# Kernel tuning notes

Measured on AMD Instinct MI355X. Metric: run time of the kernel, lower is better.

## Reference

```python
import jax, jax.numpy as jnp
import numpy as np

SX = 512; SY = 512; C = 3; NK = 10; R = 10
DT = 0.2; DD = 5; SIGMA = 0.65; THETA_A = 1.0; NPOW = 2


def setup_inputs() -> dict:
    rng = np.random.RandomState(0)
    r = rng.uniform(0.3, 1.0, NK).astype(np.float32)
    m = rng.uniform(0.05, 0.5, NK).astype(np.float32)
    s = rng.uniform(0.01, 0.18, NK).astype(np.float32)
    h = rng.uniform(0.2, 1.0, NK).astype(np.float32)
    a = rng.uniform(0.0, 1.0, (NK, 3)).astype(np.float32)
    w = rng.uniform(0.01, 0.5, (NK, 3)).astype(np.float32)
    b = rng.uniform(0.0, 1.0, (NK, 3)).astype(np.float32)
    # compute_kernel(): radial distance grid, ring sigmoid * sum-of-bumps ker_f, normalized
    mid = SX // 2
    x = np.linspace(-mid, mid, 2 * mid, dtype=np.float32)
    X, Y = np.meshgrid(x, x, indexing='ij')
    dist = np.sqrt(X ** 2 + Y ** 2)
    D = dist[:, :, None] / ((R + 15.0) * r)                      # (SX, SY, NK)
    ring = 1.0 / (1.0 + np.exp((D - 1.0) * 10.0))                # sigmoid(-(D-1)*10)
    bumps = (b * np.exp(-((D[..., None] - a) ** 2) / w)).sum(-1)  # ker_f(D, a, w, b)
    K = (ring * bumps).astype(np.float32)
    nK_ker = K / K.sum(axis=(0, 1), keepdims=True)               # (SX, SY, NK)
    # kernel -> source channel, and kernel -> target channel one-hot (c1 as matrix)
    c0 = np.array([0, 0, 0, 1, 1, 1, 2, 2, 2, 0], dtype=np.int32)
    tgt = np.array([0, 1, 2, 0, 1, 2, 0, 1, 2, 0], dtype=np.int32)
    c1_mat = np.zeros((NK, C), dtype=np.int32)
    c1_mat[np.arange(NK), tgt] = 1
    key = jax.random.key(0)
    A = jax.random.uniform(key, (SX, SY, C), dtype=jnp.float32)  # scale_init_state = 1
    return {"A": A, "nK_ker": jnp.asarray(nK_ker), "m": jnp.asarray(m),
            "s": jnp.asarray(s), "h": jnp.asarray(h),
            "c0": jnp.asarray(c0), "c1_mat": jnp.asarray(c1_mat)}


def _sobel(A):
    """A: (SX, SY, Cc) -> (SX, SY, 2, Cc), circular (toroidal) boundary."""
    def grad_ax(ax):
        sm_ax = 1 - ax
        sm = jnp.roll(A, 1, sm_ax) + 2.0 * A + jnp.roll(A, -1, sm_ax)  # [1,2,1] smoothing
        return (jnp.roll(sm, -1, ax) - jnp.roll(sm, 1, ax)) / 8.0       # central diff
    return jnp.stack([grad_ax(0), grad_ax(1)], axis=2)


def _flowlenia_step(A, nK_ker, m, s, h, c0, c1_mat):
    # FFT Lenia convolution
    fA = jnp.fft.fft2(A, axes=(0, 1))                              # (SX, SY, C) complex
    fK = jnp.fft.fft2(jnp.fft.fftshift(nK_ker, axes=(0, 1)), axes=(0, 1))
    U = jnp.real(jnp.fft.ifft2(fK * fA[:, :, c0], axes=(0, 1)))    # (SX, SY, NK)
    # growth * h, then gather-sum kernels into target channels (c1)
    U = (2.0 * jnp.exp(-((U - m) ** 2) / (2.0 * s ** 2)) - 1.0) * h
    U = jnp.einsum('xyk,kc->xyc', U, c1_mat.astype(U.dtype))       # (SX, SY, C)
    # flow field
    nabla_U = _sobel(U)                                            # (SX, SY, 2, C)
    nabla_A = _sobel(A.sum(-1, keepdims=True))                     # (SX, SY, 2, 1)
    alpha = jnp.clip((A[:, :, None, :] / THETA_A) ** NPOW, 0.0, 1.0)
    F = nabla_U * (1.0 - alpha) - nabla_A * alpha                  # (SX, SY, 2, C)
    # reintegration tracking (mass-conserving advection over (2*DD+1)^2 shifts)
    xs = jnp.arange(SX, dtype=A.dtype)
    ys = jnp.arange(SY, dtype=A.dtype)
    X, Y = jnp.meshgrid(xs, ys, indexing='ij')
    pos = jnp.stack([X, Y], axis=-1) + 0.5                         # (SX, SY, 2) cell centers
    ma = DD - SIGMA                                                # max flow magnitude
    mu = pos[..., None] + DT * jnp.clip(F, -ma, ma)                # (SX, SY, 2, C)
    shifts = jnp.array([(dx, dy) for dx in range(-DD, DD + 1)
                        for dy in range(-DD, DD + 1)], dtype=jnp.int32)
    clip_hi = min(1.0, 2.0 * SIGMA)
    inv_norm = 1.0 / (4.0 * SIGMA ** 2)

    def body(acc, sh):
        dx, dy = sh[0], sh[1]
        rA = jnp.roll(jnp.roll(A, dx, 0), dy, 1)
        rmu = jnp.roll(jnp.roll(mu, dx, 0), dy, 1)
        sz = 0.5 - jnp.abs(pos[..., None] - rmu) + SIGMA
        area = jnp.prod(jnp.clip(sz, 0.0, clip_hi), axis=2) * inv_norm  # (SX, SY, C)
        return acc + rA * area, None

    nA, _ = jax.lax.scan(body, jnp.zeros_like(A), shifts)
    return nA


def reference(A, nK_ker, m, s, h, c0, c1_mat):
    return _flowlenia_step(A, nK_ker, m, s, h, c0, c1_mat)
```

## Files before the change

### kernel.cpp

```cpp
#include <hip/hip_runtime.h>
#include <math.h>

#define NF 512
#define NF2 (NF * NF)
#define RPB 4
#define ROWLEN 580
#define PI_F 3.14159265358979323846f

#define LPAD(q) ((q) + ((q) >> 3))

__device__ inline float2 cadd(float2 a, float2 b) { return make_float2(a.x + b.x, a.y + b.y); }
__device__ inline float2 csub(float2 a, float2 b) { return make_float2(a.x - b.x, a.y - b.y); }
__device__ inline float2 cmul(float2 a, float2 b) {
    return make_float2(a.x * b.x - a.y * b.y, a.x * b.y + a.y * b.x);
}

__device__ inline void fft8(float2 x[8], float dsign) {
    const float s = 0.70710678118654752440f;
    float2 a0 = cadd(x[0], x[4]), a1 = cadd(x[1], x[5]);
    float2 a2 = cadd(x[2], x[6]), a3 = cadd(x[3], x[7]);
    float2 b0 = csub(x[0], x[4]), b1 = csub(x[1], x[5]);
    float2 b2 = csub(x[2], x[6]), b3 = csub(x[3], x[7]);
    b1 = cmul(b1, make_float2(s, dsign * s));
    b2 = make_float2(-dsign * b2.y, dsign * b2.x);
    b3 = cmul(b3, make_float2(-s, dsign * s));
    float2 c0 = cadd(a0, a2), c1 = cadd(a1, a3);
    float2 c2 = csub(a0, a2), c3 = csub(a1, a3);
    c3 = make_float2(-dsign * c3.y, dsign * c3.x);
    float2 d0 = cadd(b0, b2), d1 = cadd(b1, b3);
    float2 d2 = csub(b0, b2), d3 = csub(b1, b3);
    d3 = make_float2(-dsign * d3.y, dsign * d3.x);
    x[0] = cadd(c0, c1); x[4] = csub(c0, c1);
    x[2] = cadd(c2, c3); x[6] = csub(c2, c3);
    x[1] = cadd(d0, d1); x[5] = csub(d0, d1);
    x[3] = cadd(d2, d3); x[7] = csub(d2, d3);
}

__device__ inline void twiddle8(float2 x[8], float2 wb) {
    float2 tw = wb;
    x[1] = cmul(x[1], tw); tw = cmul(tw, wb);
    x[2] = cmul(x[2], tw); tw = cmul(tw, wb);
    x[3] = cmul(x[3], tw); tw = cmul(tw, wb);
    x[4] = cmul(x[4], tw); tw = cmul(tw, wb);
    x[5] = cmul(x[5], tw); tw = cmul(tw, wb);
    x[6] = cmul(x[6], tw); tw = cmul(tw, wb);
    x[7] = cmul(x[7], tw);
}

__device__ inline void fft512_regs(float2 x[8], int b, float2* bufA, float2* bufB,
                                   const float2* Wt, float dsign) {
    fft8(x, dsign);
    float2 wb0 = make_float2(Wt[b].x, dsign * Wt[b].y);
    twiddle8(x, wb0);
#pragma unroll
    for (int p = 0; p < 8; ++p) bufA[9 * b + p] = x[p];
    __syncthreads();
#pragma unroll
    for (int j = 0; j < 8; ++j) x[j] = bufA[LPAD(b + 64 * j)];
    fft8(x, dsign);
    int u = b >> 3, v = b & 7;
    float2 wb1 = make_float2(Wt[b & ~7].x, dsign * Wt[b & ~7].y);
    twiddle8(x, wb1);
    int base = u * 64 + v;
#pragma unroll
    for (int p = 0; p < 8; ++p) bufB[LPAD(base + 8 * p)] = x[p];
    __syncthreads();
#pragma unroll
    for (int j = 0; j < 8; ++j) x[j] = bufB[LPAD(b + 64 * j)];
    fft8(x, dsign);
}

#define FFT_PRE                                                    \
    __shared__ float2 SHA[RPB][ROWLEN];                            \
    __shared__ float2 SHB[RPB][ROWLEN];                            \
    __shared__ float2 Wt[512];                                     \
    int tid = threadIdx.x;                                         \
    int rr_ = tid >> 6, bb_ = tid & 63;                            \
    {                                                              \
        float sn, cs;                                              \
        sincosf((PI_F / 256.0f) * (float)tid, &sn, &cs);           \
        Wt[tid] = make_float2(cs, sn);                             \
        sincosf((PI_F / 256.0f) * (float)(tid + 256), &sn, &cs);   \
        Wt[tid + 256] = make_float2(cs, sn);                       \
    }

__device__ inline float2 unpack_field(const float2* __restrict__ Z, int plane, int slot,
                                      int ky, int kx) {
    const float2* P = Z + (size_t)plane * NF2;
    float2 zr = P[(ky << 9) + kx];
    float2 zm = P[(((NF - ky) & (NF - 1)) << 9) + ((NF - kx) & (NF - 1))];
    if (slot == 0)
        return make_float2(0.5f * (zr.x + zm.x), 0.5f * (zr.y - zm.y));
    else
        return make_float2(0.5f * (zr.y + zm.y), 0.5f * (zm.x - zr.x));
}

__global__ __launch_bounds__(256) void k_fwd_p1(const float* __restrict__ A,
                                                const float* __restrict__ K,
                                                float2* __restrict__ Z) {
    FFT_PRE
    int pl = blockIdx.y;
    const float* bre; int sre, cre;
    const float* bim; int sim, cim;
    switch (pl) {
        case 0: bre = A; sre = 3; cre = 0; bim = A; sim = 3; cim = 1; break;
        case 1: bre = A; sre = 3; cre = 2; bim = K; sim = 10; cim = 0; break;
        case 2: bre = K; sre = 10; cre = 1; bim = K; sim = 10; cim = 2; break;
        case 3: bre = K; sre = 10; cre = 3; bim = K; sim = 10; cim = 4; break;
        case 4: bre = K; sre = 10; cre = 5; bim = K; sim = 10; cim = 6; break;
        case 5: bre = K; sre = 10; cre = 7; bim = K; sim = 10; cim = 8; break;
        default: bre = K; sre = 10; cre = 9; bim = nullptr; sim = 0; cim = 0; break;
    }
    int x0 = blockIdx.x * RPB;
    int row = x0 + rr_;
    float2 x[8];
#pragma unroll
    for (int j = 0; j < 8; ++j) {
        int idx = (row << 9) + bb_ + 64 * j;
        float vr = bre[idx * sre + cre];
        float vi = bim ? bim[idx * sim + cim] : 0.0f;
        x[j] = make_float2(vr, vi);
    }
    __syncthreads();
    fft512_regs(x, bb_, &SHA[rr_][0], &SHB[rr_][0], Wt, -1.0f);
#pragma unroll
    for (int p2 = 0; p2 < 8; ++p2) SHA[rr_][LPAD(64 * p2 + bb_)] = x[p2];
    __syncthreads();
    for (int i = tid; i < RPB * NF; i += 256) {
        int r2 = i & (RPB - 1), ky = i >> 2;
        Z[(size_t)((pl << 9) + ky) * NF + x0 + r2] = SHA[r2][LPAD(ky)];
    }
}

__global__ __launch_bounds__(256) void k_fft_rows(float2* __restrict__ data, float dsign) {
    FFT_PRE
    int R0 = blockIdx.x * RPB;
    size_t rowbase = (size_t)(R0 + rr_) * NF;
    float2 x[8];
#pragma unroll
    for (int j = 0; j < 8; ++j) x[j] = data[rowbase + bb_ + 64 * j];
    __syncthreads();
    fft512_regs(x, bb_, &SHA[rr_][0], &SHB[rr_][0], Wt, dsign);
#pragma unroll
    for (int p2 = 0; p2 < 8; ++p2) SHA[rr_][LPAD(64 * p2 + bb_)] = x[p2];
    __syncthreads();
    for (int i = tid; i < RPB * NF; i += 256) {
        int r2 = i >> 9, xx = i & (NF - 1);
        data[(size_t)(R0 + r2) * NF + xx] = SHA[r2][LPAD(xx)];
    }
}

__global__ __launch_bounds__(256) void k_mulinv_p1(const float2* __restrict__ Z,
                                                   const int* __restrict__ c0,
                                                   float2* __restrict__ tmp) {
    FFT_PRE
    int jp = blockIdx.y;
    int k1 = 2 * jp, k2 = 2 * jp + 1;
    int pK1 = (k1 == 0) ? 1 : 2 + ((k1 - 1) >> 1);
    int sK1 = (k1 == 0) ? 1 : ((k1 - 1) & 1);
    int pK2 = 2 + ((k2 - 1) >> 1);
    int sK2 = (k2 - 1) & 1;
    int cA1 = c0[k1], cA2 = c0[k2];
    int pA1 = cA1 >> 1, sA1 = cA1 & 1;
    int pA2 = cA2 >> 1, sA2 = cA2 & 1;
    bool sameA = (cA1 == cA2);

    int ky0 = blockIdx.x * RPB;
    int ky = ky0 + rr_;
    float2 x[8];
#pragma unroll
    for (int jj = 0; jj < 8; ++jj) {
        int kx = bb_ + 64 * jj;
        float2 fk1 = unpack_field(Z, pK1, sK1, ky, kx);
        float2 fk2 = unpack_field(Z, pK2, sK2, ky, kx);
        float2 fa1 = unpack_field(Z, pA1, sA1, ky, kx);
        float2 fa2 = sameA ? fa1 : unpack_field(Z, pA2, sA2, ky, kx);
        float t1x = fk1.x * fa1.x - fk1.y * fa1.y;
        float t1y = fk1.x * fa1.y + fk1.y * fa1.x;
        float t2x = fk2.x * fa2.x - fk2.y * fa2.y;
        float t2y = fk2.x * fa2.y + fk2.y * fa2.x;
        float sgn = ((kx + ky) & 1) ? -1.0f : 1.0f;
        x[jj] = make_float2((t1x - t2y) * sgn, (t1y + t2x) * sgn);
    }
    __syncthreads();
    fft512_regs(x, bb_, &SHA[rr_][0], &SHB[rr_][0], Wt, +1.0f);
#pragma unroll
    for (int p2 = 0; p2 < 8; ++p2) SHA[rr_][LPAD(64 * p2 + bb_)] = x[p2];
    __syncthreads();
    for (int i = tid; i < RPB * NF; i += 256) {
        int r2 = i & (RPB - 1), xx = i >> 2;
        tmp[(size_t)(jp * NF + xx) * NF + ky0 + r2] = SHA[r2][LPAD(xx)];
    }
}

__global__ __launch_bounds__(256) void k_inv_p2g(const float2* __restrict__ tmp,
                                                 const float* __restrict__ mm,
                                                 const float* __restrict__ ss,
                                                 const float* __restrict__ hh,
                                                 float* __restrict__ G) {
    FFT_PRE
    int jp = blockIdx.y;
    int k1 = 2 * jp, k2 = 2 * jp + 1;
    int x0 = blockIdx.x * RPB;
    int row = x0 + rr_;
    size_t base = (size_t)(jp * NF + row) * NF;
    float2 x[8];
#pragma unroll
    for (int j2 = 0; j2 < 8; ++j2) x[j2] = tmp[base + bb_ + 64 * j2];
    __syncthreads();
    fft512_regs(x, bb_, &SHA[rr_][0], &SHB[rr_][0], Wt, +1.0f);
    float m1 = mm[k1], s1 = ss[k1], h1 = hh[k1];
    float m2 = mm[k2], s2 = ss[k2], h2 = hh[k2];
    float i2s1 = 1.0f / (2.0f * s1 * s1);
    float i2s2 = 1.0f / (2.0f * s2 * s2);
    const float scale = 1.0f / ((float)NF * (float)NF);
#pragma unroll
    for (int p2 = 0; p2 < 8; ++p2) {
        int y = 64 * p2 + bb_;
        float u1 = x[p2].x * scale, u2 = x[p2].y * scale;
        float d1 = u1 - m1, d2 = u2 - m2;
        size_t o = (size_t)row * NF + y;
        G[(size_t)k1 * NF2 + o] = (2.0f * expf(-d1 * d1 * i2s1) - 1.0f) * h1;
        G[(size_t)k2 * NF2 + o] = (2.0f * expf(-d2 * d2 * i2s2) - 1.0f) * h2;
    }
}

#define HT 38
#define HT2 (HT * HT)
#define CT 36
#define CT2 (CT * CT)
__global__ __launch_bounds__(256) void k_tail(const float* __restrict__ G,
                                              const int* __restrict__ c1,
                                              const float* __restrict__ A,
                                              float* __restrict__ out) {
    __shared__ float sUp[3][HT2];
    __shared__ float sAs[HT2];
    __shared__ float sA[3][HT2];
    __shared__ float sM[6][CT2];
    int tid = threadIdx.x;
    int X0 = blockIdx.x * 32, Y0 = blockIdx.y * 32;

    float w0[10], w1[10], w2[10];
#pragma unroll
    for (int k = 0; k < 10; ++k) {
        w0[k] = (float)c1[k * 3 + 0];
        w1[k] = (float)c1[k * 3 + 1];
        w2[k] = (float)c1[k * 3 + 2];
    }

    for (int i = tid; i < HT2; i += 256) {
        int lx = i / HT, ly = i - lx * HT;
        int xg = (X0 - 3 + lx) & (NF - 1);
        int yg = (Y0 - 3 + ly) & (NF - 1);
        int gid = xg * NF + yg;
        float a0 = 0.f, a1 = 0.f, a2 = 0.f;
#pragma unroll
        for (int k = 0; k < 10; ++k) {
            float g = G[(size_t)k * NF2 + gid];
            a0 += g * w0[k]; a1 += g * w1[k]; a2 += g * w2[k];
        }
        sUp[0][i] = a0; sUp[1][i] = a1; sUp[2][i] = a2;
        float A0 = A[gid * 3 + 0], A1 = A[gid * 3 + 1], A2 = A[gid * 3 + 2];
        sA[0][i] = A0; sA[1][i] = A1; sA[2][i] = A2;
        sAs[i] = A0 + A1 + A2;
    }
    __syncthreads();

    for (int i = tid; i < CT2; i += 256) {
        int lx = i / CT, ly = i - lx * CT;
        int ci = (lx + 1) * HT + (ly + 1);
        int xg = (X0 - 2 + lx) & (NF - 1);
        int yg = (Y0 - 2 + ly) & (NF - 1);

        auto grad38 = [&](const float* f, float& gx, float& gy) {
            float fmm = f[ci - HT - 1], fm0 = f[ci - HT], fmp = f[ci - HT + 1];
            float f0m = f[ci - 1], f0p = f[ci + 1];
            float fpm = f[ci + HT - 1], fp0 = f[ci + HT], fpp = f[ci + HT + 1];
            gx = (fpm + 2.0f * fp0 + fpp - fmm - 2.0f * fm0 - fmp) * 0.125f;
            gy = (fmp + 2.0f * f0p + fpp - fmm - 2.0f * f0m - fpm) * 0.125f;
        };
        float gax, gay;
        grad38(sAs, gax, gay);
        float px = (float)xg + 0.5f, py = (float)yg + 0.5f;
#pragma unroll
        for (int c = 0; c < 3; ++c) {
            float gux, guy;
            grad38(sUp[c], gux, guy);
            float a = sA[c][ci];
            float al = fminf(a * a, 1.0f);
            float Fx = gux * (1.0f - al) - gax * al;
            float Fy = guy * (1.0f - al) - gay * al;
            Fx = fminf(fmaxf(Fx, -4.35f), 4.35f);
            Fy = fminf(fmaxf(Fy, -4.35f), 4.35f);
            sM[c][i] = px + 0.2f * Fx;
            sM[3 + c][i] = py + 0.2f * Fy;
        }
    }
    __syncthreads();

    const float INV_NORM = (float)(1.0 / (4.0 * 0.65 * 0.65));
    int cy = tid & 31, cx0 = tid >> 5;
    for (int sidx = 0; sidx < 4; ++sidx) {
        int cx = cx0 + 8 * sidx;
        int x = X0 + cx, y = Y0 + cy;
        float px = (float)x + 0.5f, py = (float)y + 0.5f;
        float acc0 = 0.f, acc1 = 0.f, acc2 = 0.f;
#pragma unroll
        for (int dx = 0; dx < 5; ++dx)
#pragma unroll
            for (int dy = 0; dy < 5; ++dy) {
                int li36 = (cx + dx) * CT + (cy + dy);
                int li38 = (cx + dx + 1) * HT + (cy + dy + 1);
#pragma unroll
                for (int c = 0; c < 3; ++c) {
                    float mux = sM[c][li36], muy = sM[3 + c][li36];
                    float szx = 0.5f - fabsf(px - mux) + 0.65f;
                    float szy = 0.5f - fabsf(py - muy) + 0.65f;
                    szx = fminf(fmaxf(szx, 0.0f), 1.0f);
                    szy = fminf(fmaxf(szy, 0.0f), 1.0f);
                    float area = szx * szy * INV_NORM;
                    float v = sA[c][li38] * area;
                    if (c == 0) acc0 += v;
                    else if (c == 1) acc1 += v;
                    else acc2 += v;
                }
            }
        int gid = x * NF + y;
        out[gid * 3 + 0] = acc0;
        out[gid * 3 + 1] = acc1;
        out[gid * 3 + 2] = acc2;
    }
}

extern "C" void kernel_launch(void* const* d_in, const int* in_sizes, int n_in,
                              void* d_out, int out_size, void* d_ws, size_t ws_size,
                              hipStream_t stream) {
    (void)in_sizes; (void)n_in; (void)out_size; (void)ws_size;
    const float* A  = (const float*)d_in[0];
    const float* nK = (const float*)d_in[1];
    const float* m  = (const float*)d_in[2];
    const float* s  = (const float*)d_in[3];
    const float* h  = (const float*)d_in[4];
    const int*   c0 = (const int*)d_in[5];
    const int*   c1 = (const int*)d_in[6];
    float* out = (float*)d_out;

    char* ws = (char*)d_ws;
    float2* Z   = (float2*)ws;
    float2* tmp = (float2*)(ws + 14680064);
    float*  G   = (float*)ws;

    dim3 blk(256);
    k_fwd_p1<<<dim3(NF / RPB, 7), blk, 0, stream>>>(A, nK, Z);
    k_fft_rows<<<dim3(7 * NF / RPB), blk, 0, stream>>>(Z, -1.0f);
    k_mulinv_p1<<<dim3(NF / RPB, 5), blk, 0, stream>>>(Z, c0, tmp);
    k_inv_p2g<<<dim3(NF / RPB, 5),   blk, 0, stream>>>(tmp, m, s, h, G);
    k_tail<<<dim3(16, 16), blk, 0, stream>>>(G, c1, A, out);
}
```

Measured before the change: 135.0 us.

## Fuse second forward FFT pass with spectral multiply and first inverse pass

Merges the forward row FFT, the spectrum unpack/multiply and the first inverse FFT pass into one kernel. Each block handles a conjugate-symmetric pair of rows (b and NF-b) across all 7 planes and keeps them in shared memory, so the Z round trip through global memory and one launch disappear. The inverse second pass now reads transposed data with float4 loads into shared memory and transposes there instead of in global writes. The cost is large shared memory per block and only 256 blocks of 512 threads, which limits occupancy, plus a special case for the self-conjugate rows 0 and 256.

```diff
diff --git a/kernel.cpp b/kernel.cpp
--- a/kernel.cpp
+++ b/kernel.cpp
@@ -84,17 +84,6 @@
         Wt[tid + 256] = make_float2(cs, sn);                       \
     }
 
-__device__ inline float2 unpack_field(const float2* __restrict__ Z, int plane, int slot,
-                                      int ky, int kx) {
-    const float2* P = Z + (size_t)plane * NF2;
-    float2 zr = P[(ky << 9) + kx];
-    float2 zm = P[(((NF - ky) & (NF - 1)) << 9) + ((NF - kx) & (NF - 1))];
-    if (slot == 0)
-        return make_float2(0.5f * (zr.x + zm.x), 0.5f * (zr.y - zm.y));
-    else
-        return make_float2(0.5f * (zr.y + zm.y), 0.5f * (zm.x - zr.x));
-}
-
 __global__ __launch_bounds__(256) void k_fwd_p1(const float* __restrict__ A,
                                                 const float* __restrict__ K,
                                                 float2* __restrict__ Z) {
@@ -132,94 +121,141 @@
     }
 }
 
-__global__ __launch_bounds__(256) void k_fft_rows(float2* __restrict__ data, float dsign) {
-    FFT_PRE
-    int R0 = blockIdx.x * RPB;
-    size_t rowbase = (size_t)(R0 + rr_) * NF;
-    float2 x[8];
-#pragma unroll
-    for (int j = 0; j < 8; ++j) x[j] = data[rowbase + bb_ + 64 * j];
-    __syncthreads();
-    fft512_regs(x, bb_, &SHA[rr_][0], &SHB[rr_][0], Wt, dsign);
-#pragma unroll
-    for (int p2 = 0; p2 < 8; ++p2) SHA[rr_][LPAD(64 * p2 + bb_)] = x[p2];
-    __syncthreads();
-    for (int i = tid; i < RPB * NF; i += 256) {
-        int r2 = i >> 9, xx = i & (NF - 1);
-        data[(size_t)(R0 + r2) * NF + xx] = SHA[r2][LPAD(xx)];
-    }
-}
-
-__global__ __launch_bounds__(256) void k_mulinv_p1(const float2* __restrict__ Z,
-                                                   const int* __restrict__ c0,
-                                                   float2* __restrict__ tmp) {
-    FFT_PRE
-    int jp = blockIdx.y;
-    int k1 = 2 * jp, k2 = 2 * jp + 1;
-    int pK1 = (k1 == 0) ? 1 : 2 + ((k1 - 1) >> 1);
-    int sK1 = (k1 == 0) ? 1 : ((k1 - 1) & 1);
-    int pK2 = 2 + ((k2 - 1) >> 1);
-    int sK2 = (k2 - 1) & 1;
-    int cA1 = c0[k1], cA2 = c0[k2];
-    int pA1 = cA1 >> 1, sA1 = cA1 & 1;
-    int pA2 = cA2 >> 1, sA2 = cA2 & 1;
-    bool sameA = (cA1 == cA2);
-
-    int ky0 = blockIdx.x * RPB;
-    int ky = ky0 + rr_;
-    float2 x[8];
-#pragma unroll
-    for (int jj = 0; jj < 8; ++jj) {
-        int kx = bb_ + 64 * jj;
-        float2 fk1 = unpack_field(Z, pK1, sK1, ky, kx);
-        float2 fk2 = unpack_field(Z, pK2, sK2, ky, kx);
-        float2 fa1 = unpack_field(Z, pA1, sA1, ky, kx);
-        float2 fa2 = sameA ? fa1 : unpack_field(Z, pA2, sA2, ky, kx);
-        float t1x = fk1.x * fa1.x - fk1.y * fa1.y;
-        float t1y = fk1.x * fa1.y + fk1.y * fa1.x;
-        float t2x = fk2.x * fa2.x - fk2.y * fa2.y;
-        float t2y = fk2.x * fa2.y + fk2.y * fa2.x;
-        float sgn = ((kx + ky) & 1) ? -1.0f : 1.0f;
-        x[jj] = make_float2((t1x - t2y) * sgn, (t1y + t2x) * sgn);
-    }
-    __syncthreads();
-    fft512_regs(x, bb_, &SHA[rr_][0], &SHB[rr_][0], Wt, +1.0f);
-#pragma unroll
-    for (int p2 = 0; p2 < 8; ++p2) SHA[rr_][LPAD(64 * p2 + bb_)] = x[p2];
-    __syncthreads();
-    for (int i = tid; i < RPB * NF; i += 256) {
-        int r2 = i & (RPB - 1), xx = i >> 2;
-        tmp[(size_t)(jp * NF + xx) * NF + ky0 + r2] = SHA[r2][LPAD(xx)];
-    }
-}
-
-__global__ __launch_bounds__(256) void k_inv_p2g(const float2* __restrict__ tmp,
+__global__ __launch_bounds__(512) void k_rows_mul(const float2* __restrict__ Z,
+                                                  const int* __restrict__ c0,
+                                                  float2* __restrict__ tmpT) {
+    __shared__ float2 RS[14][NF];
+    __shared__ float2 SCA[8][ROWLEN];
+    __shared__ float2 SCB[8][ROWLEN];
+    __shared__ float2 Wt[512];
+    int tid = threadIdx.x;
+    int rr_ = tid >> 6, bb_ = tid & 63;
+    {
+        float sn, cs;
+        sincosf((PI_F / 256.0f) * (float)tid, &sn, &cs);
+        Wt[tid] = make_float2(cs, sn);
+    }
+    int b = blockIdx.x;
+    bool selfm = (b == 0);
+    int r1 = selfm ? 0 : b;
+    int r2 = selfm ? 256 : NF - b;
+    __syncthreads();
+
+    for (int batch = 0; batch < 2; ++batch) {
+        int ridx = batch * 8 + rr_;
+        int rc = ridx < 14 ? ridx : 13;
+        int p = rc >> 1, sl = rc & 1;
+        int row = sl ? r2 : r1;
+        float2 x[8];
+        size_t base = (size_t)((p << 9) + row) * NF;
+#pragma unroll
+        for (int jj = 0; jj < 8; ++jj) x[jj] = Z[base + bb_ + 64 * jj];
+        fft512_regs(x, bb_, &SCA[rr_][0], &SCB[rr_][0], Wt, -1.0f);
+        if (ridx < 14) {
+#pragma unroll
+            for (int pp = 0; pp < 8; ++pp) RS[ridx][64 * pp + bb_] = x[pp];
+        }
+    }
+    __syncthreads();
+
+    for (int batch = 0; batch < 2; ++batch) {
+        int q = batch * 8 + rr_;
+        int qc = q < 10 ? q : 8;
+        int j = qc >> 1, sl = qc & 1;
+        int k1 = 2 * j, k2 = 2 * j + 1;
+        int pK1 = (k1 == 0) ? 1 : 2 + ((k1 - 1) >> 1);
+        int sK1 = (k1 == 0) ? 1 : ((k1 - 1) & 1);
+        int pK2 = 2 + ((k2 - 1) >> 1);
+        int sK2 = (k2 - 1) & 1;
+        int cA1 = c0[k1], cA2 = c0[k2];
+        int pA1 = cA1 >> 1, sA1 = cA1 & 1;
+        int pA2 = cA2 >> 1, sA2 = cA2 & 1;
+        int mo = selfm ? sl : (1 - sl);
+        float2 x[8];
+#pragma unroll
+        for (int jj = 0; jj < 8; ++jj) {
+            int kx = bb_ + 64 * jj;
+            int mkx = (NF - kx) & (NF - 1);
+            float2 zr, zm, fk1, fk2, fa1, fa2;
+            zr = RS[2 * pK1 + sl][kx]; zm = RS[2 * pK1 + mo][mkx];
+            fk1 = sK1 == 0 ? make_float2(0.5f * (zr.x + zm.x), 0.5f * (zr.y - zm.y))
+                           : make_float2(0.5f * (zr.y + zm.y), 0.5f * (zm.x - zr.x));
+            zr = RS[2 * pK2 + sl][kx]; zm = RS[2 * pK2 + mo][mkx];
+            fk2 = sK2 == 0 ? make_float2(0.5f * (zr.x + zm.x), 0.5f * (zr.y - zm.y))
+                           : make_float2(0.5f * (zr.y + zm.y), 0.5f * (zm.x - zr.x));
+            zr = RS[2 * pA1 + sl][kx]; zm = RS[2 * pA1 + mo][mkx];
+            fa1 = sA1 == 0 ? make_float2(0.5f * (zr.x + zm.x), 0.5f * (zr.y - zm.y))
+                           : make_float2(0.5f * (zr.y + zm.y), 0.5f * (zm.x - zr.x));
+            if (cA2 == cA1) fa2 = fa1;
+            else {
+                zr = RS[2 * pA2 + sl][kx]; zm = RS[2 * pA2 + mo][mkx];
+                fa2 = sA2 == 0 ? make_float2(0.5f * (zr.x + zm.x), 0.5f * (zr.y - zm.y))
+                               : make_float2(0.5f * (zr.y + zm.y), 0.5f * (zm.x - zr.x));
+            }
+            float t1x = fk1.x * fa1.x - fk1.y * fa1.y;
+            float t1y = fk1.x * fa1.y + fk1.y * fa1.x;
+            float t2x = fk2.x * fa2.x - fk2.y * fa2.y;
+            float t2y = fk2.x * fa2.y + fk2.y * fa2.x;
+            float sgn = ((kx + b) & 1) ? -1.0f : 1.0f;
+            x[jj] = make_float2((t1x - t2y) * sgn, (t1y + t2x) * sgn);
+        }
+        fft512_regs(x, bb_, &SCA[rr_][0], &SCB[rr_][0], Wt, +1.0f);
+        if (q < 10) {
+            int orow = sl ? r2 : r1;
+            size_t obase = ((size_t)j * NF + orow) * NF;
+#pragma unroll
+            for (int pp = 0; pp < 8; ++pp) tmpT[obase + 64 * pp + bb_] = x[pp];
+        }
+    }
+}
+
+__global__ __launch_bounds__(256) void k_inv_p2g(const float2* __restrict__ tmpT,
                                                  const float* __restrict__ mm,
                                                  const float* __restrict__ ss,
                                                  const float* __restrict__ hh,
                                                  float* __restrict__ G) {
-    FFT_PRE
-    int jp = blockIdx.y;
-    int k1 = 2 * jp, k2 = 2 * jp + 1;
-    int x0 = blockIdx.x * RPB;
-    int row = x0 + rr_;
-    size_t base = (size_t)(jp * NF + row) * NF;
+    __shared__ float2 SH[4][NF];
+    __shared__ float2 SCA[4][ROWLEN];
+    __shared__ float2 SCB[4][ROWLEN];
+    __shared__ float2 Wt[512];
+    int tid = threadIdx.x;
+    int rr_ = tid >> 6, bb_ = tid & 63;
+    {
+        float sn, cs;
+        sincosf((PI_F / 256.0f) * (float)tid, &sn, &cs);
+        Wt[tid] = make_float2(cs, sn);
+        sincosf((PI_F / 256.0f) * (float)(tid + 256), &sn, &cs);
+        Wt[tid + 256] = make_float2(cs, sn);
+    }
+    int j = blockIdx.y;
+    int x0 = blockIdx.x * 4;
+    for (int t = tid; t < NF; t += 256) {
+        const float2* src = tmpT + ((size_t)j * NF + t) * NF + x0;
+        float4 v0 = *(const float4*)(src);
+        float4 v1 = *(const float4*)(src + 2);
+        SH[0][t] = make_float2(v0.x, v0.y);
+        SH[1][t] = make_float2(v0.z, v0.w);
+        SH[2][t] = make_float2(v1.x, v1.y);
+        SH[3][t] = make_float2(v1.z, v1.w);
+    }
+    __syncthreads();
     float2 x[8];
 #pragma unroll
-    for (int j2 = 0; j2 < 8; ++j2) x[j2] = tmp[base + bb_ + 64 * j2];
-    __syncthreads();
-    fft512_regs(x, bb_, &SHA[rr_][0], &SHB[rr_][0], Wt, +1.0f);
+    for (int jj = 0; jj < 8; ++jj) x[jj] = SH[rr_][bb_ + 64 * jj];
+    fft512_regs(x, bb_, &SCA[rr_][0], &SCB[rr_][0], Wt, +1.0f);
+    int k1 = 2 * j, k2 = 2 * j + 1;
     float m1 = mm[k1], s1 = ss[k1], h1 = hh[k1];
     float m2 = mm[k2], s2 = ss[k2], h2 = hh[k2];
     float i2s1 = 1.0f / (2.0f * s1 * s1);
     float i2s2 = 1.0f / (2.0f * s2 * s2);
     const float scale = 1.0f / ((float)NF * (float)NF);
+    int xcol = x0 + rr_;
 #pragma unroll
     for (int p2 = 0; p2 < 8; ++p2) {
         int y = 64 * p2 + bb_;
         float u1 = x[p2].x * scale, u2 = x[p2].y * scale;
         float d1 = u1 - m1, d2 = u2 - m2;
-        size_t o = (size_t)row * NF + y;
+        size_t o = (size_t)xcol * NF + y;
         G[(size_t)k1 * NF2 + o] = (2.0f * expf(-d1 * d1 * i2s1) - 1.0f) * h1;
         G[(size_t)k2 * NF2 + o] = (2.0f * expf(-d2 * d2 * i2s2) - 1.0f) * h2;
     }
@@ -346,14 +382,12 @@
     float* out = (float*)d_out;
 
     char* ws = (char*)d_ws;
-    float2* Z   = (float2*)ws;
-    float2* tmp = (float2*)(ws + 14680064);
-    float*  G   = (float*)ws;
-
-    dim3 blk(256);
-    k_fwd_p1<<<dim3(NF / RPB, 7), blk, 0, stream>>>(A, nK, Z);
-    k_fft_rows<<<dim3(7 * NF / RPB), blk, 0, stream>>>(Z, -1.0f);
-    k_mulinv_p1<<<dim3(NF / RPB, 5), blk, 0, stream>>>(Z, c0, tmp);
-    k_inv_p2g<<<dim3(NF / RPB, 5),   blk, 0, stream>>>(tmp, m, s, h, G);
-    k_tail<<<dim3(16, 16), blk, 0, stream>>>(G, c1, A, out);
-}
+    float2* Z    = (float2*)ws;
+    float2* tmpT = (float2*)(ws + 14680064);
+    float*  G    = (float*)ws;
+
+    k_fwd_p1<<<dim3(NF / RPB, 7), dim3(256), 0, stream>>>(A, nK, Z);
+    k_rows_mul<<<dim3(256), dim3(512), 0, stream>>>(Z, c0, tmpT);
+    k_inv_p2g<<<dim3(NF / 4, 5), dim3(256), 0, stream>>>(tmpT, m, s, h, G);
+    k_tail<<<dim3(16, 16), dim3(256), 0, stream>>>(G, c1, A, out);
+}
```

Result: faster. 130.0 us (-3.7%).
